# Performance work log

Measured on AMD Instinct MI355X. Metric: run time of the kernel, lower is better.

Reference implementation:

```python
import jax, jax.numpy as jnp
import numpy as np

B, T, C, H = 8, 2048, 768, 64  # batch, block_size, n_embd, head_size

def setup_inputs() -> dict:
    key = jax.random.key(0)
    kx, kk, kq, kv = jax.random.split(key, 4)
    x = jax.random.normal(kx, (B, T, C), dtype=jnp.float32)
    Wk = jax.random.normal(kk, (C, H), dtype=jnp.float32) * (C ** -0.5)
    Wq = jax.random.normal(kq, (C, H), dtype=jnp.float32) * (C ** -0.5)
    Wv = jax.random.normal(kv, (C, H), dtype=jnp.float32) * (C ** -0.5)
    return {"x": x, "Wk": Wk, "Wq": Wq, "Wv": Wv}

def reference(x, Wk, Wq, Wv):
    # single causal self-attention head (dropout in eval mode = identity)
    k = jnp.einsum('btc,ch->bth', x, Wk)  # [B,T,H]
    q = jnp.einsum('btc,ch->bth', x, Wq)
    v = jnp.einsum('btc,ch->bth', x, Wv)
    scale = jnp.asarray(k.shape[-1], x.dtype) ** -0.5
    wei = jnp.einsum('bth,bsh->bts', q, k) * scale  # [B,T,T]
    t = x.shape[1]
    causal = jnp.tril(jnp.ones((t, t), dtype=bool))
    wei = jnp.where(causal[None, :, :], wei, jnp.asarray(-jnp.inf, wei.dtype))
    wei = jax.nn.softmax(wei, axis=-1)
    out = jnp.einsum('bts,bsh->bth', wei, v)  # [B,T,H]
    return out
```

## Files before the change

kernel.cpp:

```cpp
#include <hip/hip_runtime.h>
#include <hip/hip_bf16.h>

typedef __attribute__((ext_vector_type(8))) short short8;
typedef __attribute__((ext_vector_type(4))) float f32x4;

#define B_  8
#define T_  2048
#define C_  768
#define H_  64
#define M_  (B_ * T_)

#define GLDS16(g, l) __builtin_amdgcn_global_load_lds(                        \
    (const __attribute__((address_space(1))) void*)(g),                       \
    (__attribute__((address_space(3))) void*)(l), 16, 0, 0)

static __device__ __forceinline__ unsigned short f2bf(float f) {
    __hip_bfloat16 h = __float2bfloat16(f);
    return *reinterpret_cast<unsigned short*>(&h);
}

static __device__ __forceinline__ short8 make_frag(const unsigned short* p0, const unsigned short* p1) {
    const ushort4 a = *reinterpret_cast<const ushort4*>(p0);
    const ushort4 b = *reinterpret_cast<const ushort4*>(p1);
    short8 r;
    r[0] = (short)a.x; r[1] = (short)a.y; r[2] = (short)a.z; r[3] = (short)a.w;
    r[4] = (short)b.x; r[5] = (short)b.y; r[6] = (short)b.z; r[7] = (short)b.w;
    return r;
}

static __device__ __forceinline__ int swz(int row, int u) {
    return row * 64 + ((((u) >> 3) ^ (row & 7)) << 3) + (u & 7);
}

static __device__ __forceinline__ int fragoff(int k) {
    const int half = k >> 5;
    const int kk   = k & 31;
    const int c    = half * 4 + ((kk >> 2) & 3);
    const int p    = (kk & 3) + ((kk & 16) >> 2);
    return c * 8 + p;
}

#define LOG2E_SCALE 0.18033688011112042f

__global__ __launch_bounds__(256) void prep_w(
    const float* __restrict__ Wq, const float* __restrict__ Wk, const float* __restrict__ Wv,
    unsigned short* __restrict__ Wt) {

    const int t   = threadIdx.x;
    const int mat = blockIdx.x / 48;
    const int kb  = blockIdx.x % 48;
    const int h   = t & 63;
    const int k0  = (kb * 4 + (t >> 6)) * 4;

    const float* Ws = (mat == 0) ? Wq : (mat == 1) ? Wk : Wv;
    const float sc  = (mat == 0) ? LOG2E_SCALE : 1.f;
    ushort4 o;
    o.x = f2bf(Ws[(size_t)(k0 + 0) * H_ + h] * sc);
    o.y = f2bf(Ws[(size_t)(k0 + 1) * H_ + h] * sc);
    o.z = f2bf(Ws[(size_t)(k0 + 2) * H_ + h] * sc);
    o.w = f2bf(Ws[(size_t)(k0 + 3) * H_ + h] * sc);
    *reinterpret_cast<ushort4*>(&Wt[(size_t)(mat * 64 + h) * C_ + k0]) = o;
}

__global__ __launch_bounds__(256) void proj_kernel(
    const float* __restrict__ x, const unsigned short* __restrict__ Wt,
    unsigned short* __restrict__ qkv) {

    __shared__ unsigned short Als[4 * 12 * 512];

    const int tid = threadIdx.x;
    const int w   = tid >> 6;
    const int l   = tid & 63;
    const int lg  = l >> 4;
    const int lc  = l & 15;
    const int row0 = blockIdx.x * 64;

    const int sr   = tid >> 2;
    const int so   = tid & 3;
    const int srt  = sr >> 4;
    const int sr15 = sr & 15;
    const int sbase = (so * 16 + (sr15 ^ so)) * 8;

    f32x4 acc[4][3];
#pragma unroll
    for (int rt = 0; rt < 4; ++rt)
#pragma unroll
        for (int ct = 0; ct < 3; ++ct) acc[rt][ct] = (f32x4)0.f;

    const unsigned short* bbase[3];
#pragma unroll
    for (int ct = 0; ct < 3; ++ct)
        bbase[ct] = Wt + (size_t)(w * 48 + ct * 16 + lc) * C_ + lg * 8;

    for (int phase = 0; phase < 2; ++phase) {
        if (phase) __syncthreads();
#pragma unroll
        for (int g = 0; g < 3; ++g) {
            float4 fa[4][2];
#pragma unroll
            for (int jj = 0; jj < 4; ++jj) {
                const int j = g * 4 + jj;
                const float* xp = x + (size_t)(row0 + sr) * C_ + phase * 384 + j * 32 + so * 8;
                fa[jj][0] = *reinterpret_cast<const float4*>(xp);
                fa[jj][1] = *reinterpret_cast<const float4*>(xp + 4);
            }
#pragma unroll
            for (int jj = 0; jj < 4; ++jj) {
                const int j = g * 4 + jj;
                short8 v;
                v[0] = (short)f2bf(fa[jj][0].x); v[1] = (short)f2bf(fa[jj][0].y);
                v[2] = (short)f2bf(fa[jj][0].z); v[3] = (short)f2bf(fa[jj][0].w);
                v[4] = (short)f2bf(fa[jj][1].x); v[5] = (short)f2bf(fa[jj][1].y);
                v[6] = (short)f2bf(fa[jj][1].z); v[7] = (short)f2bf(fa[jj][1].w);
                *reinterpret_cast<short8*>(&Als[(srt * 12 + j) * 512 + sbase]) = v;
            }
        }
        __syncthreads();

        short8 bcur[3], bnxt[3];
#pragma unroll
        for (int ct = 0; ct < 3; ++ct)
            bcur[ct] = *reinterpret_cast<const short8*>(bbase[ct] + phase * 384);

#pragma unroll
        for (int kk = 0; kk < 12; ++kk) {
            if (kk < 11) {
#pragma unroll
                for (int ct = 0; ct < 3; ++ct)
                    bnxt[ct] = *reinterpret_cast<const short8*>(bbase[ct] + phase * 384 + (kk + 1) * 32);
            }
            short8 af[4];
#pragma unroll
            for (int rt = 0; rt < 4; ++rt)
                af[rt] = *reinterpret_cast<const short8*>(
                    &Als[(rt * 12 + kk) * 512 + (lg * 16 + (lc ^ lg)) * 8]);
#pragma unroll
            for (int rt = 0; rt < 4; ++rt)
#pragma unroll
                for (int ct = 0; ct < 3; ++ct)
                    acc[rt][ct] = __builtin_amdgcn_mfma_f32_16x16x32_bf16(af[rt], bcur[ct], acc[rt][ct], 0, 0, 0);
            if (kk < 11) {
#pragma unroll
                for (int ct = 0; ct < 3; ++ct) bcur[ct] = bnxt[ct];
            }
        }
    }

    unsigned short* Qd   = qkv;
    unsigned short* Kimg = qkv + (size_t)M_ * H_;
    unsigned short* Vimg = qkv + (size_t)2 * M_ * H_;
    const size_t g12 = (size_t)blockIdx.x << 12;
#pragma unroll
    for (int ct = 0; ct < 3; ++ct) {
        const int col = w * 48 + ct * 16 + lc;
        const int mat = col >> 6;
        const int h   = col & 63;
        const int foh = fragoff(h);
#pragma unroll
        for (int rt = 0; rt < 4; ++rt)
#pragma unroll
            for (int j = 0; j < 4; ++j) {
                const int s6 = rt * 16 + lg * 4 + j;
                const unsigned short v = f2bf(acc[rt][ct][j]);
                if (mat == 0)      Qd[(size_t)(row0 + s6) * H_ + h] = v;
                else if (mat == 1) Kimg[g12 + swz(s6, foh)] = v;
                else               Vimg[g12 + swz(h, fragoff(s6))] = v;
            }
    }
}

#define SEG_FLOATS 4224

template<int SEG>
static __device__ __forceinline__ int segs_per_batch() { return SEG == 32 ? 32 : 80; }

template<int SEG>
static __device__ __forceinline__ void decode_seg(int r, int& qt, int& seg) {
    if (SEG == 32) { qt = r; seg = 0; return; }
    if (r < 8)       { qt = r;                seg = 0; }
    else if (r < 24) { qt = 8  + (r - 8) / 2; seg = (r - 8) & 1; }
    else if (r < 48) { qt = 16 + (r - 24) / 3; seg = (r - 24) % 3; }
    else             { qt = 24 + (r - 48) / 4; seg = (r - 48) & 3; }
}

template<int SEG>
static __device__ __forceinline__ int seg_prefix(int qt) {
    if (SEG == 32) return qt;
    if (qt < 8)  return qt;
    if (qt < 16) return 8  + 2 * (qt - 8);
    if (qt < 24) return 24 + 3 * (qt - 16);
    return 48 + 4 * (qt - 24);
}

template<int SEG>
__global__ __launch_bounds__(256) void attn_partial(
    const unsigned short* __restrict__ qkv, float* __restrict__ part,
    float* __restrict__ out) {

    const int spb = segs_per_batch<SEG>();
    const int b   = blockIdx.x / spb;
    const int rr  = spb - 1 - (blockIdx.x % spb);
    int qt, seg;
    decode_seg<SEG>(rr, qt, seg);

    const int tid = threadIdx.x;
    const int w  = tid >> 6;
    const int l  = tid & 63;
    const int lg = l >> 4;
    const int lc = l & 15;

    __shared__ unsigned short Kls[2][4096];
    __shared__ unsigned short Vls[2][4096];

    const unsigned short* Qg = qkv;
    const unsigned short* Kg = qkv + (size_t)M_ * H_;
    const unsigned short* Vg = qkv + (size_t)2 * M_ * H_;

    const unsigned short* qrow = Qg + (size_t)(b * T_ + qt * 64 + w * 16 + lc) * H_;
    short8 qf[2];
#pragma unroll
    for (int ks = 0; ks < 2; ++ks)
        qf[ks] = make_frag(qrow + ks * 32 + lg * 4, qrow + ks * 32 + lg * 4 + 16);

    float mval = -1e30f, lsum = 0.f;
    f32x4 oT[4];
#pragma unroll
    for (int t = 0; t < 4; ++t) oT[t] = (f32x4)0.f;

    const int q_glob = qt * 64 + w * 16 + lc;

    const int kv_beg = seg * SEG;
    const int kv_end = min(kv_beg + SEG, qt + 1);

    const int go = w * 1024 + l * 8;

    auto stage = [&](int buf, int kv) {
        const size_t tb = ((size_t)(b * 32 + kv)) << 12;
        const unsigned short* kt = Kg + tb;
        const unsigned short* vt = Vg + tb;
        GLDS16(kt + go,       &Kls[buf][w * 1024]);
        GLDS16(kt + go + 512, &Kls[buf][w * 1024 + 512]);
        GLDS16(vt + go,       &Vls[buf][w * 1024]);
        GLDS16(vt + go + 512, &Vls[buf][w * 1024 + 512]);
    };

    stage(0, kv_beg);
    int cur = 0;

    for (int kv = kv_beg; kv < kv_end; ++kv) {
        const bool more = (kv + 1 < kv_end);
        __builtin_amdgcn_s_barrier();
        asm volatile("" ::: "memory");
        if (more) {
            stage(cur ^ 1, kv + 1);
            asm volatile("s_waitcnt vmcnt(4)" ::: "memory");
        } else {
            asm volatile("s_waitcnt vmcnt(0)" ::: "memory");
        }
        __builtin_amdgcn_s_barrier();
        asm volatile("" ::: "memory");

        const unsigned short* Kc = Kls[cur];
        const unsigned short* Vc = Vls[cur];

        f32x4 sT[4];
#pragma unroll
        for (int st = 0; st < 4; ++st) {
            f32x4 accs = (f32x4)0.f;
#pragma unroll
            for (int ks = 0; ks < 2; ++ks) {
                const short8 kf = *reinterpret_cast<const short8*>(
                    &Kc[swz(st * 16 + lc, (ks * 4 + lg) * 8)]);
                accs = __builtin_amdgcn_mfma_f32_16x16x32_bf16(kf, qf[ks], accs, 0, 0, 0);
            }
            sT[st] = accs;
        }

        float p[4][4];
#pragma unroll
        for (int st = 0; st < 4; ++st)
#pragma unroll
            for (int r = 0; r < 4; ++r)
                p[st][r] = sT[st][r];

        if (kv == qt) {
#pragma unroll
            for (int st = 0; st < 4; ++st)
#pragma unroll
                for (int r = 0; r < 4; ++r)
                    if ((kv * 64 + st * 16 + lg * 4 + r) > q_glob) p[st][r] = -1e30f;
        }

        float pm[4];
#pragma unroll
        for (int st = 0; st < 4; ++st)
            pm[st] = fmaxf(fmaxf(p[st][0], p[st][1]), fmaxf(p[st][2], p[st][3]));
        float pmax = fmaxf(fmaxf(pm[0], pm[1]), fmaxf(pm[2], pm[3]));
        pmax = fmaxf(pmax, __shfl_xor(pmax, 16));
        pmax = fmaxf(pmax, __shfl_xor(pmax, 32));

        if (!__all(pmax <= mval)) {
            const float mnew  = fmaxf(mval, pmax);
            const float alpha = exp2f(mval - mnew);
            mval = mnew;
            lsum *= alpha;
#pragma unroll
            for (int ht = 0; ht < 4; ++ht) oT[ht] *= alpha;
        }

        float ps[4];
#pragma unroll
        for (int st = 0; st < 4; ++st) {
#pragma unroll
            for (int r = 0; r < 4; ++r)
                p[st][r] = exp2f(p[st][r] - mval);
            ps[st] = (p[st][0] + p[st][1]) + (p[st][2] + p[st][3]);
        }
        float srow = (ps[0] + ps[1]) + (ps[2] + ps[3]);
        srow += __shfl_xor(srow, 16);
        srow += __shfl_xor(srow, 32);
        lsum += srow;

        short8 pb[2];
#pragma unroll
        for (int ks = 0; ks < 2; ++ks) {
#pragma unroll
            for (int r = 0; r < 4; ++r) {
                pb[ks][r]     = (short)f2bf(p[2 * ks][r]);
                pb[ks][r + 4] = (short)f2bf(p[2 * ks + 1][r]);
            }
        }

#pragma unroll
        for (int ks = 0; ks < 2; ++ks) {
#pragma unroll
            for (int ht = 0; ht < 4; ++ht) {
                const short8 vf = *reinterpret_cast<const short8*>(
                    &Vc[swz(ht * 16 + lc, (ks * 4 + lg) * 8)]);
                oT[ht] = __builtin_amdgcn_mfma_f32_16x16x32_bf16(vf, pb[ks], oT[ht], 0, 0, 0);
            }
        }
        cur ^= 1;
    }

    const int nseg = (SEG == 32) ? 1 : (qt / 8 + 1);
    if (nseg == 1) {
        const float inv = 1.f / lsum;
        float* op = out + (size_t)(b * T_ + q_glob) * H_;
#pragma unroll
        for (int ht = 0; ht < 4; ++ht) {
            f32x4 v = oT[ht] * inv;
            *reinterpret_cast<f32x4*>(&op[ht * 16 + lg * 4]) = v;
        }
    } else {
        float* base = part + (size_t)(b * spb + seg_prefix<SEG>(qt) + seg) * SEG_FLOATS;
#pragma unroll
        for (int ht = 0; ht < 4; ++ht)
            *reinterpret_cast<f32x4*>(&base[(w * 16 + lc) * 64 + ht * 16 + lg * 4]) = oT[ht];
        if (lg == 0) {
            base[4096 + w * 16 + lc] = mval;
            base[4160 + w * 16 + lc] = lsum;
        }
    }
}

__global__ __launch_bounds__(256) void attn_merge8(
    const float* __restrict__ part, float* __restrict__ out) {

    const int b  = blockIdx.x / 24;
    const int qt = 8 + blockIdx.x % 24;
    const int nseg = qt / 8 + 1;
    const float* base0 = part + (size_t)(b * 80 + seg_prefix<8>(qt)) * SEG_FLOATS;

    const int tid = threadIdx.x;
    const int row = tid >> 2;
    const int c0  = (tid & 3) * 16;

    float M = -1e30f;
    for (int s = 0; s < nseg; ++s)
        M = fmaxf(M, base0[(size_t)s * SEG_FLOATS + 4096 + row]);

    float L = 0.f;
    f32x4 acc[4];
#pragma unroll
    for (int k = 0; k < 4; ++k) acc[k] = (f32x4)0.f;

    for (int s = 0; s < nseg; ++s) {
        const float* sb = base0 + (size_t)s * SEG_FLOATS;
        const float wsc = exp2f(sb[4096 + row] - M);
        L += sb[4160 + row] * wsc;
#pragma unroll
        for (int k = 0; k < 4; ++k) {
            const f32x4 ov = *reinterpret_cast<const f32x4*>(&sb[row * 64 + c0 + 4 * k]);
            acc[k] += ov * wsc;
        }
    }
    const float inv = 1.f / L;
    float* op = out + (size_t)(b * T_ + qt * 64 + row) * H_ + c0;
#pragma unroll
    for (int k = 0; k < 4; ++k)
        *reinterpret_cast<f32x4*>(&op[4 * k]) = acc[k] * inv;
}

extern "C" void kernel_launch(void* const* d_in, const int* in_sizes, int n_in,
                              void* d_out, int out_size, void* d_ws, size_t ws_size,
                              hipStream_t stream) {
    const float* x  = (const float*)d_in[0];
    const float* Wk = (const float*)d_in[1];
    const float* Wq = (const float*)d_in[2];
    const float* Wv = (const float*)d_in[3];

    const size_t qkvB = (size_t)3 * M_ * H_ * 2;
    const size_t WtB  = (size_t)3 * H_ * C_ * 2;
    unsigned short* qkv = (unsigned short*)d_ws;
    unsigned short* Wt  = (unsigned short*)((char*)d_ws + qkvB);
    float* part = (float*)((char*)d_ws + qkvB + WtB);
    float* out  = (float*)d_out;

    prep_w<<<dim3(144), dim3(256), 0, stream>>>(Wq, Wk, Wv, Wt);
    proj_kernel<<<dim3(M_ / 64), dim3(256), 0, stream>>>(x, Wt, qkv);

    const size_t need8 = qkvB + WtB + (size_t)(B_ * 80) * SEG_FLOATS * 4;
    if (ws_size >= need8) {
        attn_partial<8><<<dim3(B_ * 80), dim3(256), 0, stream>>>(qkv, part, out);
        attn_merge8<<<dim3(B_ * 24), dim3(256), 0, stream>>>(part, out);
    } else {
        attn_partial<32><<<dim3(B_ * 32), dim3(256), 0, stream>>>(qkv, part, out);
    }
}
```

Measured before the change: 55.77 us.

## Fuse split-KV merge into attention via atomic last-block, pipeline projection staging

The separate merge kernel is removed. Each partial attention block now writes its partial result, bumps a per-(batch, q-tile) atomic counter, and the last-arriving block performs the merge in place. The counters are zeroed inside prep_w. Separately, the projection kernel now stages x in six double-buffered 128-wide chunks with register prefetch instead of two 384-wide phases, which cuts LDS use and overlaps global loads with MFMA. The trade-offs are fence and atomic overhead plus a serialized merge tail, and the W-fragment prefetch was dropped in favor of per-step loads.

```diff
diff --git a/kernel.cpp b/kernel.cpp
--- a/kernel.cpp
+++ b/kernel.cpp
@@ -44,9 +44,11 @@
 
 __global__ __launch_bounds__(256) void prep_w(
     const float* __restrict__ Wq, const float* __restrict__ Wk, const float* __restrict__ Wv,
-    unsigned short* __restrict__ Wt) {
+    unsigned short* __restrict__ Wt, int* __restrict__ ctr) {
 
     const int t   = threadIdx.x;
+    if (blockIdx.x == 0) ctr[t] = 0;
+
     const int mat = blockIdx.x / 48;
     const int kb  = blockIdx.x % 48;
     const int h   = t & 63;
@@ -66,7 +68,7 @@
     const float* __restrict__ x, const unsigned short* __restrict__ Wt,
     unsigned short* __restrict__ qkv) {
 
-    __shared__ unsigned short Als[4 * 12 * 512];
+    __shared__ unsigned short Als[2][8192];
 
     const int tid = threadIdx.x;
     const int w   = tid >> 6;
@@ -92,57 +94,50 @@
     for (int ct = 0; ct < 3; ++ct)
         bbase[ct] = Wt + (size_t)(w * 48 + ct * 16 + lc) * C_ + lg * 8;
 
-    for (int phase = 0; phase < 2; ++phase) {
-        if (phase) __syncthreads();
-#pragma unroll
-        for (int g = 0; g < 3; ++g) {
-            float4 fa[4][2];
+    const float* xrow = x + (size_t)(row0 + sr) * C_ + so * 8;
+
+    float4 fa[4][2];
+#pragma unroll
+    for (int jj = 0; jj < 4; ++jj) {
+        fa[jj][0] = *reinterpret_cast<const float4*>(xrow + jj * 32);
+        fa[jj][1] = *reinterpret_cast<const float4*>(xrow + jj * 32 + 4);
+    }
+
+#pragma unroll
+    for (int c = 0; c < 6; ++c) {
+#pragma unroll
+        for (int jj = 0; jj < 4; ++jj) {
+            short8 v;
+            v[0] = (short)f2bf(fa[jj][0].x); v[1] = (short)f2bf(fa[jj][0].y);
+            v[2] = (short)f2bf(fa[jj][0].z); v[3] = (short)f2bf(fa[jj][0].w);
+            v[4] = (short)f2bf(fa[jj][1].x); v[5] = (short)f2bf(fa[jj][1].y);
+            v[6] = (short)f2bf(fa[jj][1].z); v[7] = (short)f2bf(fa[jj][1].w);
+            *reinterpret_cast<short8*>(&Als[c & 1][(srt * 4 + jj) * 512 + sbase]) = v;
+        }
+        if (c < 5) {
 #pragma unroll
             for (int jj = 0; jj < 4; ++jj) {
-                const int j = g * 4 + jj;
-                const float* xp = x + (size_t)(row0 + sr) * C_ + phase * 384 + j * 32 + so * 8;
-                fa[jj][0] = *reinterpret_cast<const float4*>(xp);
-                fa[jj][1] = *reinterpret_cast<const float4*>(xp + 4);
+                fa[jj][0] = *reinterpret_cast<const float4*>(xrow + (c + 1) * 128 + jj * 32);
+                fa[jj][1] = *reinterpret_cast<const float4*>(xrow + (c + 1) * 128 + jj * 32 + 4);
             }
-#pragma unroll
-            for (int jj = 0; jj < 4; ++jj) {
-                const int j = g * 4 + jj;
-                short8 v;
-                v[0] = (short)f2bf(fa[jj][0].x); v[1] = (short)f2bf(fa[jj][0].y);
-                v[2] = (short)f2bf(fa[jj][0].z); v[3] = (short)f2bf(fa[jj][0].w);
-                v[4] = (short)f2bf(fa[jj][1].x); v[5] = (short)f2bf(fa[jj][1].y);
-                v[6] = (short)f2bf(fa[jj][1].z); v[7] = (short)f2bf(fa[jj][1].w);
-                *reinterpret_cast<short8*>(&Als[(srt * 12 + j) * 512 + sbase]) = v;
-            }
         }
         __syncthreads();
-
-        short8 bcur[3], bnxt[3];
-#pragma unroll
-        for (int ct = 0; ct < 3; ++ct)
-            bcur[ct] = *reinterpret_cast<const short8*>(bbase[ct] + phase * 384);
-
-#pragma unroll
-        for (int kk = 0; kk < 12; ++kk) {
-            if (kk < 11) {
-#pragma unroll
-                for (int ct = 0; ct < 3; ++ct)
-                    bnxt[ct] = *reinterpret_cast<const short8*>(bbase[ct] + phase * 384 + (kk + 1) * 32);
-            }
+#pragma unroll
+        for (int kk = 0; kk < 4; ++kk) {
+            short8 bcur[3];
+#pragma unroll
+            for (int ct = 0; ct < 3; ++ct)
+                bcur[ct] = *reinterpret_cast<const short8*>(bbase[ct] + c * 128 + kk * 32);
             short8 af[4];
 #pragma unroll
             for (int rt = 0; rt < 4; ++rt)
                 af[rt] = *reinterpret_cast<const short8*>(
-                    &Als[(rt * 12 + kk) * 512 + (lg * 16 + (lc ^ lg)) * 8]);
+                    &Als[c & 1][(rt * 4 + kk) * 512 + (lg * 16 + (lc ^ lg)) * 8]);
 #pragma unroll
             for (int rt = 0; rt < 4; ++rt)
 #pragma unroll
                 for (int ct = 0; ct < 3; ++ct)
                     acc[rt][ct] = __builtin_amdgcn_mfma_f32_16x16x32_bf16(af[rt], bcur[ct], acc[rt][ct], 0, 0, 0);
-            if (kk < 11) {
-#pragma unroll
-                for (int ct = 0; ct < 3; ++ct) bcur[ct] = bnxt[ct];
-            }
         }
     }
 
@@ -195,7 +190,7 @@
 template<int SEG>
 __global__ __launch_bounds__(256) void attn_partial(
     const unsigned short* __restrict__ qkv, float* __restrict__ part,
-    float* __restrict__ out) {
+    float* __restrict__ out, int* __restrict__ ctr) {
 
     const int spb = segs_per_batch<SEG>();
     const int b   = blockIdx.x / spb;
@@ -211,6 +206,7 @@
 
     __shared__ unsigned short Kls[2][4096];
     __shared__ unsigned short Vls[2][4096];
+    __shared__ int lastFlag;
 
     const unsigned short* Qg = qkv;
     const unsigned short* Kg = qkv + (size_t)M_ * H_;
@@ -352,33 +348,35 @@
             f32x4 v = oT[ht] * inv;
             *reinterpret_cast<f32x4*>(&op[ht * 16 + lg * 4]) = v;
         }
-    } else {
-        float* base = part + (size_t)(b * spb + seg_prefix<SEG>(qt) + seg) * SEG_FLOATS;
-#pragma unroll
-        for (int ht = 0; ht < 4; ++ht)
-            *reinterpret_cast<f32x4*>(&base[(w * 16 + lc) * 64 + ht * 16 + lg * 4]) = oT[ht];
-        if (lg == 0) {
-            base[4096 + w * 16 + lc] = mval;
-            base[4160 + w * 16 + lc] = lsum;
-        }
-    }
-}
-
-__global__ __launch_bounds__(256) void attn_merge8(
-    const float* __restrict__ part, float* __restrict__ out) {
-
-    const int b  = blockIdx.x / 24;
-    const int qt = 8 + blockIdx.x % 24;
-    const int nseg = qt / 8 + 1;
-    const float* base0 = part + (size_t)(b * 80 + seg_prefix<8>(qt)) * SEG_FLOATS;
-
-    const int tid = threadIdx.x;
+        return;
+    }
+
+    float* base = part + (size_t)(b * spb + seg_prefix<SEG>(qt) + seg) * SEG_FLOATS;
+#pragma unroll
+    for (int ht = 0; ht < 4; ++ht)
+        *reinterpret_cast<f32x4*>(&base[(w * 16 + lc) * 64 + ht * 16 + lg * 4]) = oT[ht];
+    if (lg == 0) {
+        base[4096 + w * 16 + lc] = mval;
+        base[4160 + w * 16 + lc] = lsum;
+    }
+    __threadfence();
+    __syncthreads();
+    if (tid == 0) {
+        const int old = __hip_atomic_fetch_add(&ctr[b * 32 + qt], 1,
+                                               __ATOMIC_ACQ_REL, __HIP_MEMORY_SCOPE_AGENT);
+        lastFlag = (old == nseg - 1);
+    }
+    __syncthreads();
+    if (!lastFlag) return;
+    __threadfence();
+
     const int row = tid >> 2;
     const int c0  = (tid & 3) * 16;
-
-    float M = -1e30f;
+    const float* base0 = part + (size_t)(b * spb + seg_prefix<SEG>(qt)) * SEG_FLOATS;
+
+    float Mx = -1e30f;
     for (int s = 0; s < nseg; ++s)
-        M = fmaxf(M, base0[(size_t)s * SEG_FLOATS + 4096 + row]);
+        Mx = fmaxf(Mx, base0[(size_t)s * SEG_FLOATS + 4096 + row]);
 
     float L = 0.f;
     f32x4 acc[4];
@@ -387,7 +385,7 @@
 
     for (int s = 0; s < nseg; ++s) {
         const float* sb = base0 + (size_t)s * SEG_FLOATS;
-        const float wsc = exp2f(sb[4096 + row] - M);
+        const float wsc = exp2f(sb[4096 + row] - Mx);
         L += sb[4160 + row] * wsc;
 #pragma unroll
         for (int k = 0; k < 4; ++k) {
@@ -410,21 +408,22 @@
     const float* Wq = (const float*)d_in[2];
     const float* Wv = (const float*)d_in[3];
 
-    const size_t qkvB = (size_t)3 * M_ * H_ * 2;
-    const size_t WtB  = (size_t)3 * H_ * C_ * 2;
+    const size_t qkvB  = (size_t)3 * M_ * H_ * 2;
+    const size_t WtB   = (size_t)3 * H_ * C_ * 2;
+    const size_t partB = (size_t)(B_ * 80) * SEG_FLOATS * 4;
     unsigned short* qkv = (unsigned short*)d_ws;
     unsigned short* Wt  = (unsigned short*)((char*)d_ws + qkvB);
     float* part = (float*)((char*)d_ws + qkvB + WtB);
+    int*   ctr  = (int*)((char*)d_ws + qkvB + WtB + partB);
     float* out  = (float*)d_out;
 
-    prep_w<<<dim3(144), dim3(256), 0, stream>>>(Wq, Wk, Wv, Wt);
+    prep_w<<<dim3(144), dim3(256), 0, stream>>>(Wq, Wk, Wv, Wt, ctr);
     proj_kernel<<<dim3(M_ / 64), dim3(256), 0, stream>>>(x, Wt, qkv);
 
-    const size_t need8 = qkvB + WtB + (size_t)(B_ * 80) * SEG_FLOATS * 4;
+    const size_t need8 = qkvB + WtB + partB + 256 * sizeof(int);
     if (ws_size >= need8) {
-        attn_partial<8><<<dim3(B_ * 80), dim3(256), 0, stream>>>(qkv, part, out);
-        attn_merge8<<<dim3(B_ * 24), dim3(256), 0, stream>>>(part, out);
+        attn_partial<8><<<dim3(B_ * 80), dim3(256), 0, stream>>>(qkv, part, out, ctr);
     } else {
-        attn_partial<32><<<dim3(B_ * 32), dim3(256), 0, stream>>>(qkv, part, out);
-    }
-}
+        attn_partial<32><<<dim3(B_ * 32), dim3(256), 0, stream>>>(qkv, part, out, ctr);
+    }
+}
```

Measured after the change: 169.6 us. +204.1%, slower.

## Double-buffer x tiles in projection kernel to overlap loads with MFMA

Applied to the files above, without the earlier changes.

Restructures the QKV projection kernel's K loop from two 384-wide phases into six 128-wide chunks with a double-buffered LDS tile. The global loads for the next chunk of x are issued before the MFMA work on the current chunk, so memory latency can hide behind compute. LDS use drops from 48 KB to 32 KB, which may raise occupancy. There are fewer block-level barriers per chunk, and the explicit B-fragment register prefetch has been removed.

```diff
diff --git a/kernel.cpp b/kernel.cpp
--- a/kernel.cpp
+++ b/kernel.cpp
@@ -66,7 +66,7 @@
     const float* __restrict__ x, const unsigned short* __restrict__ Wt,
     unsigned short* __restrict__ qkv) {
 
-    __shared__ unsigned short Als[4 * 12 * 512];
+    __shared__ unsigned short Als[2][8192];
 
     const int tid = threadIdx.x;
     const int w   = tid >> 6;
@@ -92,57 +92,50 @@
     for (int ct = 0; ct < 3; ++ct)
         bbase[ct] = Wt + (size_t)(w * 48 + ct * 16 + lc) * C_ + lg * 8;
 
-    for (int phase = 0; phase < 2; ++phase) {
-        if (phase) __syncthreads();
-#pragma unroll
-        for (int g = 0; g < 3; ++g) {
-            float4 fa[4][2];
+    const float* xrow = x + (size_t)(row0 + sr) * C_ + so * 8;
+
+    float4 fa[4][2];
+#pragma unroll
+    for (int jj = 0; jj < 4; ++jj) {
+        fa[jj][0] = *reinterpret_cast<const float4*>(xrow + jj * 32);
+        fa[jj][1] = *reinterpret_cast<const float4*>(xrow + jj * 32 + 4);
+    }
+
+#pragma unroll
+    for (int c = 0; c < 6; ++c) {
+#pragma unroll
+        for (int jj = 0; jj < 4; ++jj) {
+            short8 v;
+            v[0] = (short)f2bf(fa[jj][0].x); v[1] = (short)f2bf(fa[jj][0].y);
+            v[2] = (short)f2bf(fa[jj][0].z); v[3] = (short)f2bf(fa[jj][0].w);
+            v[4] = (short)f2bf(fa[jj][1].x); v[5] = (short)f2bf(fa[jj][1].y);
+            v[6] = (short)f2bf(fa[jj][1].z); v[7] = (short)f2bf(fa[jj][1].w);
+            *reinterpret_cast<short8*>(&Als[c & 1][(srt * 4 + jj) * 512 + sbase]) = v;
+        }
+        if (c < 5) {
 #pragma unroll
             for (int jj = 0; jj < 4; ++jj) {
-                const int j = g * 4 + jj;
-                const float* xp = x + (size_t)(row0 + sr) * C_ + phase * 384 + j * 32 + so * 8;
-                fa[jj][0] = *reinterpret_cast<const float4*>(xp);
-                fa[jj][1] = *reinterpret_cast<const float4*>(xp + 4);
+                fa[jj][0] = *reinterpret_cast<const float4*>(xrow + (c + 1) * 128 + jj * 32);
+                fa[jj][1] = *reinterpret_cast<const float4*>(xrow + (c + 1) * 128 + jj * 32 + 4);
             }
-#pragma unroll
-            for (int jj = 0; jj < 4; ++jj) {
-                const int j = g * 4 + jj;
-                short8 v;
-                v[0] = (short)f2bf(fa[jj][0].x); v[1] = (short)f2bf(fa[jj][0].y);
-                v[2] = (short)f2bf(fa[jj][0].z); v[3] = (short)f2bf(fa[jj][0].w);
-                v[4] = (short)f2bf(fa[jj][1].x); v[5] = (short)f2bf(fa[jj][1].y);
-                v[6] = (short)f2bf(fa[jj][1].z); v[7] = (short)f2bf(fa[jj][1].w);
-                *reinterpret_cast<short8*>(&Als[(srt * 12 + j) * 512 + sbase]) = v;
-            }
         }
         __syncthreads();
-
-        short8 bcur[3], bnxt[3];
-#pragma unroll
-        for (int ct = 0; ct < 3; ++ct)
-            bcur[ct] = *reinterpret_cast<const short8*>(bbase[ct] + phase * 384);
-
-#pragma unroll
-        for (int kk = 0; kk < 12; ++kk) {
-            if (kk < 11) {
-#pragma unroll
-                for (int ct = 0; ct < 3; ++ct)
-                    bnxt[ct] = *reinterpret_cast<const short8*>(bbase[ct] + phase * 384 + (kk + 1) * 32);
-            }
+#pragma unroll
+        for (int kk = 0; kk < 4; ++kk) {
+            short8 bcur[3];
+#pragma unroll
+            for (int ct = 0; ct < 3; ++ct)
+                bcur[ct] = *reinterpret_cast<const short8*>(bbase[ct] + c * 128 + kk * 32);
             short8 af[4];
 #pragma unroll
             for (int rt = 0; rt < 4; ++rt)
                 af[rt] = *reinterpret_cast<const short8*>(
-                    &Als[(rt * 12 + kk) * 512 + (lg * 16 + (lc ^ lg)) * 8]);
+                    &Als[c & 1][(rt * 4 + kk) * 512 + (lg * 16 + (lc ^ lg)) * 8]);
 #pragma unroll
             for (int rt = 0; rt < 4; ++rt)
 #pragma unroll
                 for (int ct = 0; ct < 3; ++ct)
                     acc[rt][ct] = __builtin_amdgcn_mfma_f32_16x16x32_bf16(af[rt], bcur[ct], acc[rt][ct], 0, 0, 0);
-            if (kk < 11) {
-#pragma unroll
-                for (int ct = 0; ct < 3; ++ct) bcur[ct] = bnxt[ct];
-            }
         }
     }
 
```

After: 56.12 us. About the same (+0.6%).
